# Performance work log

Hardware: AMD Instinct MI355X
Metric: run time of the kernel (lower is better)

## Reference

```python
import jax, jax.numpy as jnp
import numpy as np

N_U, N_I, E = 500000, 50000, 1000000
H, C = 4, 32  # heads, per-head channels


def _seg_softmax(e, dst, n_dst):
    # e: [E, H] edge scores, softmax over edges sharing the same destination
    m = jax.ops.segment_max(e, dst, num_segments=n_dst)
    ex = jnp.exp(e - m[dst])
    s = jax.ops.segment_sum(ex, dst, num_segments=n_dst)
    return ex / (s[dst] + 1e-16)


def _gatv2(xl, xr, src, dst, att, bias, n_dst, edge_feat=None):
    # GATv2 bipartite message passing (PyG semantics, no self-loops for bipartite).
    # xl: [N_src,H,C] transformed source, xr: [N_dst,H,C] transformed destination
    h = xl[src] + xr[dst]                      # [E,H,C] gather + add
    if edge_feat is not None:
        h = h + edge_feat                      # [E,H,C]
    e = jnp.sum(jax.nn.leaky_relu(h, 0.2) * att, axis=-1)   # [E,H]
    alpha = _seg_softmax(e, dst, n_dst)                      # [E,H]
    out = jax.ops.segment_sum(alpha[..., None] * xl[src], dst, num_segments=n_dst)
    return out.reshape(n_dst, H * C) + bias    # concat heads + bias


def setup_inputs() -> dict:
    key = jax.random.key(0)
    ks = iter(jax.random.split(key, 32))
    p = lambda *s: jax.random.normal(next(ks), s, dtype=jnp.float32) * 0.05
    inp = {
        "customer_x": jax.random.normal(next(ks), (N_U, 101), dtype=jnp.float32),
        "fund_x": jax.random.normal(next(ks), (N_I, 1), dtype=jnp.float32),
        "edge_attr": jax.random.uniform(next(ks), (E, 3), dtype=jnp.float32),
        "edge_src": jax.random.randint(next(ks), (E,), 0, N_U),
        "edge_dst": jax.random.randint(next(ks), (E,), 0, N_I),
        # input projections
        "user_W": p(101, 32), "user_b": jnp.zeros((32,), jnp.float32),
        "item_W": p(1, 32),   "item_b": jnp.zeros((32,), jnp.float32),
        # conv1: GATv2Conv((32,32), 32, heads=4, edge_dim=3)
        "c1_Wl": p(32, H * C), "c1_bl": jnp.zeros((H * C,), jnp.float32),
        "c1_Wr": p(32, H * C), "c1_br": jnp.zeros((H * C,), jnp.float32),
        "c1_We": p(3, H * C),
        "c1_att": p(H, C), "c1_bias": jnp.zeros((H * C,), jnp.float32),
        # conv2: GATv2Conv((128,32), 32, heads=4), called without edge_attr
        "c2_Wl": p(H * C, H * C), "c2_bl": jnp.zeros((H * C,), jnp.float32),
        "c2_Wr": p(32, H * C),    "c2_br": jnp.zeros((H * C,), jnp.float32),
        "c2_att": p(H, C), "c2_bias": jnp.zeros((H * C,), jnp.float32),
        # classifier MLP: 128 -> 64 -> 1
        "cls_W1": p(128, 64), "cls_b1": jnp.zeros((64,), jnp.float32),
        "cls_W2": p(64, 1),   "cls_b2": jnp.zeros((1,), jnp.float32),
    }
    return inp


def reference(customer_x, fund_x, edge_attr, edge_src, edge_dst,
              user_W, user_b, item_W, item_b,
              c1_Wl, c1_bl, c1_Wr, c1_br, c1_We, c1_att, c1_bias,
              c2_Wl, c2_bl, c2_Wr, c2_br, c2_att, c2_bias,
              cls_W1, cls_b1, cls_W2, cls_b2):
    user_x = customer_x @ user_W + user_b            # [N_U,32]
    item_x = fund_x @ item_W + item_b                # [N_I,32]
    # conv1: customer -> fund (dst = fund)
    xl1 = (user_x @ c1_Wl + c1_bl).reshape(N_U, H, C)
    xr1 = (item_x @ c1_Wr + c1_br).reshape(N_I, H, C)
    ef1 = (edge_attr @ c1_We).reshape(E, H, C)
    item_h = jax.nn.relu(_gatv2(xl1, xr1, edge_src, edge_dst, c1_att, c1_bias, N_I, ef1))
    # conv2: fund -> customer (edge_index flipped, no edge_attr)
    xl2 = (item_h @ c2_Wl + c2_bl).reshape(N_I, H, C)
    xr2 = (user_x @ c2_Wr + c2_br).reshape(N_U, H, C)
    user_h = _gatv2(xl2, xr2, edge_dst, edge_src, c2_att, c2_bias, N_U)  # [N_U,128]
    # anomaly classifier
    hid = jax.nn.relu(user_h @ cls_W1 + cls_b1)
    scores = jax.nn.sigmoid(hid @ cls_W2 + cls_b2)   # [N_U,1]
    return scores
```

## Files before the change

kernel.cpp:

```cpp
#include <hip/hip_runtime.h>
#include <cstdint>
#include <cstddef>

#define NU 500000
#define NI 50000
#define NE 1000000
#define HC 128
#define NH 4

typedef __attribute__((ext_vector_type(8))) short bf16x8;
typedef __attribute__((ext_vector_type(4))) float f32x4;

union frag_u { bf16x8 v; unsigned int u[4]; };

__device__ __forceinline__ unsigned int pack_bf2(float x, float y) {
    unsigned int r;
    asm("v_cvt_pk_bf16_f32 %0, %1, %2" : "=v"(r) : "v"(x), "v"(y));
    return r;
}
__device__ __forceinline__ float2 unpack_bf2(unsigned int v) {
    return make_float2(__uint_as_float(v << 16),
                       __uint_as_float(v & 0xffff0000u));
}
__device__ __forceinline__ unsigned short pack_bf1(float x) {
    unsigned int b = __float_as_uint(x);
    b += 0x7fffu + ((b >> 16) & 1u);
    return (unsigned short)(b >> 16);
}

__device__ __forceinline__ float head_reduce(float p) {
    p += __shfl_xor(p, 8, 16);
    p += __shfl_xor(p, 4, 16);
    p += __shfl_xor(p, 2, 16);
    p += __shfl_xor(p, 1, 16);
    return p;
}

__global__ void wprep(const float* __restrict__ user_W, const float* __restrict__ user_b,
                      const float* __restrict__ c1_Wl, const float* __restrict__ c1_bl,
                      const float* __restrict__ c2_Wr, const float* __restrict__ c2_br,
                      const float* __restrict__ c2_Wl, unsigned short* __restrict__ Bp)
{
    const int t = blockIdx.x * 256 + threadIdx.x;
    const int mat = t >> 14;
    const int k = (t >> 7) & 127;
    const int n = t & 127;
    float val = 0.f;
    if (mat == 2) {
        val = c2_Wl[k * 128 + n];
    } else {
        const float* W2 = mat ? c2_Wr : c1_Wl;
        if (k < 101) {
            for (int q = 0; q < 32; ++q) val = fmaf(user_W[k * 32 + q], W2[q * 128 + n], val);
        } else if (k == 101) {
            for (int q = 0; q < 32; ++q) val = fmaf(user_b[q], W2[q * 128 + n], val);
            val += (mat ? c2_br : c1_bl)[n];
        }
    }
    const int fi = (mat * 8 + (n >> 4)) * 4 + (k >> 5);
    const int lane_ = (n & 15) + ((k >> 3) & 3) * 16;
    Bp[(size_t)fi * 512 + lane_ * 8 + (k & 7)] = pack_bf1(val);
}

__global__ void w1prep(const float* __restrict__ W1, unsigned short* __restrict__ Bp1)
{
    const int t = blockIdx.x * 256 + threadIdx.x;
    const int k = t >> 6;
    const int n = t & 63;
    const float val = W1[k * 64 + n];
    const int fi = (n >> 4) * 4 + (k >> 5);
    const int lane_ = (n & 15) + ((k >> 3) & 3) * 16;
    Bp1[(size_t)fi * 512 + lane_ * 8 + (k & 7)] = pack_bf1(val);
}

__global__ void wvbb_prep(const float* __restrict__ item_W, const float* __restrict__ item_b,
                          const float* __restrict__ c1_Wr, const float* __restrict__ c1_br,
                          float* __restrict__ wvbb)
{
    const int j = threadIdx.x;
    if (j >= 128) return;
    float wv = 0.f, bb = 0.f;
    for (int q = 0; q < 32; ++q) {
        wv = fmaf(item_W[q], c1_Wr[q * 128 + j], wv);
        bb = fmaf(item_b[q], c1_Wr[q * 128 + j], bb);
    }
    wvbb[j] = wv;
    wvbb[128 + j] = bb + c1_br[j];
}

__global__ __launch_bounds__(256)
void mfma_user_scatter(const float* __restrict__ cx, const unsigned short* __restrict__ Bp,
                       unsigned short* __restrict__ outL, unsigned short* __restrict__ outR,
                       int M, int nub,
                       const int* __restrict__ src, const int* __restrict__ dst,
                       const float* __restrict__ eattr,
                       const int* __restrict__ offU, const int* __restrict__ offI,
                       const int* __restrict__ rankU, const int* __restrict__ rankI,
                       int* __restrict__ sFund, uint4* __restrict__ sE1, int E, int nscat)
{
    __shared__ float xs[64 * 108];

    if (blockIdx.x < nscat) {
        const int bid = blockIdx.x;
        for (int i = bid * 256 + threadIdx.x; i < E; i += nscat * 256) {
            const int s = src[i];
            const int d = dst[i];
            const float a0 = eattr[3 * (size_t)i];
            const float a1 = eattr[3 * (size_t)i + 1];
            const float a2 = eattr[3 * (size_t)i + 2];
            const int p1 = offI[d] + rankI[i];
            const int p2 = offU[s] + rankU[i];
            sE1[p1] = make_uint4((unsigned int)s, __float_as_uint(a0),
                                 __float_as_uint(a1), __float_as_uint(a2));
            sFund[p2] = d;
        }
        return;
    }

    const int tid = threadIdx.x;
    const int lane = tid & 63;
    const int wid = tid >> 6;
    const int rowblk = (blockIdx.x - nscat) * 64;
    const int rows = min(64, M - rowblk);

    const float* srcp = cx + (size_t)rowblk * 101;
    const int total = rows * 101;
    for (int i = tid; i < total; i += 256) {
        const int r = i / 101;
        const int c = i - r * 101;
        xs[r * 108 + c] = srcp[i];
    }
    __syncthreads();

    const int rowbase = wid * 16;
    if (rowbase >= rows) return;
    const int row = lane & 15;
    const int chunk = lane >> 4;
    const float* rowp = xs + (rowbase + row) * 108;

    frag_u a[4];
    #pragma unroll
    for (int ks = 0; ks < 3; ++ks) {
        const int kb = ks * 32 + chunk * 8;
        const float4 p = *(const float4*)(rowp + kb);
        const float4 q = *(const float4*)(rowp + kb + 4);
        a[ks].u[0] = pack_bf2(p.x, p.y);
        a[ks].u[1] = pack_bf2(p.z, p.w);
        a[ks].u[2] = pack_bf2(q.x, q.y);
        a[ks].u[3] = pack_bf2(q.z, q.w);
    }
    {
        float v0 = 0.f, v1 = 0.f, v2 = 0.f, v3 = 0.f, v4 = 0.f, v5 = 0.f;
        if (chunk == 0) {
            const float4 p = *(const float4*)(rowp + 96);
            v0 = p.x; v1 = p.y; v2 = p.z; v3 = p.w;
            v4 = rowp[100];
            v5 = 1.0f;
        }
        a[3].u[0] = pack_bf2(v0, v1);
        a[3].u[1] = pack_bf2(v2, v3);
        a[3].u[2] = pack_bf2(v4, v5);
        a[3].u[3] = 0u;
    }

    unsigned short* xpo = (unsigned short*)(xs + (size_t)wid * 16 * 108);

    const bf16x8* bfr = (const bf16x8*)Bp;
    #pragma unroll
    for (int mat = 0; mat < 2; ++mat) {
        unsigned short* outp = mat ? outR : outL;
        #pragma unroll
        for (int nf = 0; nf < 8; ++nf) {
            f32x4 acc = {0.f, 0.f, 0.f, 0.f};
            const int fi = (mat * 8 + nf) * 4;
            acc = __builtin_amdgcn_mfma_f32_16x16x32_bf16(a[0].v, bfr[(fi + 0) * 64 + lane], acc, 0, 0, 0);
            acc = __builtin_amdgcn_mfma_f32_16x16x32_bf16(a[1].v, bfr[(fi + 1) * 64 + lane], acc, 0, 0, 0);
            acc = __builtin_amdgcn_mfma_f32_16x16x32_bf16(a[2].v, bfr[(fi + 2) * 64 + lane], acc, 0, 0, 0);
            acc = __builtin_amdgcn_mfma_f32_16x16x32_bf16(a[3].v, bfr[(fi + 3) * 64 + lane], acc, 0, 0, 0);
            const int col = nf * 16 + row;
            #pragma unroll
            for (int j = 0; j < 4; ++j)
                xpo[(chunk * 4 + j) * 140 + col] = pack_bf1(acc[j]);
        }
        #pragma unroll
        for (int i = 0; i < 4; ++i) {
            const int r = i * 4 + chunk;
            const bf16x8 v = *(const bf16x8*)&xpo[r * 140 + row * 8];
            *(bf16x8*)(outp + (size_t)(rowblk + rowbase + r) * 128 + row * 8) = v;
        }
    }
}

__global__ __launch_bounds__(256)
void mfma_xl2(const float* __restrict__ X, const unsigned short* __restrict__ Bp,
              const float* __restrict__ bias, unsigned short* __restrict__ outp, int M)
{
    const int lane = threadIdx.x & 63;
    const int wt = (blockIdx.x * blockDim.x + threadIdx.x) >> 6;
    const int rowbase = wt * 16;
    if (rowbase >= M) return;
    const int chunk = lane >> 4;
    const float* rowp = X + (size_t)(rowbase + (lane & 15)) * 128;

    frag_u a[4];
    #pragma unroll
    for (int ks = 0; ks < 4; ++ks) {
        const int kb = ks * 32 + chunk * 8;
        const float4 p = *(const float4*)(rowp + kb);
        const float4 q = *(const float4*)(rowp + kb + 4);
        a[ks].u[0] = pack_bf2(p.x, p.y);
        a[ks].u[1] = pack_bf2(p.z, p.w);
        a[ks].u[2] = pack_bf2(q.x, q.y);
        a[ks].u[3] = pack_bf2(q.z, q.w);
    }

    const bf16x8* bfr = (const bf16x8*)Bp;
    #pragma unroll
    for (int nf = 0; nf < 8; ++nf) {
        f32x4 acc = {0.f, 0.f, 0.f, 0.f};
        const int fi = (16 + nf) * 4;
        acc = __builtin_amdgcn_mfma_f32_16x16x32_bf16(a[0].v, bfr[(fi + 0) * 64 + lane], acc, 0, 0, 0);
        acc = __builtin_amdgcn_mfma_f32_16x16x32_bf16(a[1].v, bfr[(fi + 1) * 64 + lane], acc, 0, 0, 0);
        acc = __builtin_amdgcn_mfma_f32_16x16x32_bf16(a[2].v, bfr[(fi + 2) * 64 + lane], acc, 0, 0, 0);
        acc = __builtin_amdgcn_mfma_f32_16x16x32_bf16(a[3].v, bfr[(fi + 3) * 64 + lane], acc, 0, 0, 0);
        const int col = nf * 16 + (lane & 15);
        const float bv = bias[col];
        #pragma unroll
        for (int j = 0; j < 4; ++j)
            outp[(size_t)(rowbase + chunk * 4 + j) * 128 + col] = pack_bf1(acc[j] + bv);
    }
}

__global__ void hist_rank(const int* __restrict__ src, const int* __restrict__ dst,
                          int* __restrict__ cntU, int* __restrict__ cntI,
                          int* __restrict__ rankU, int* __restrict__ rankI, int E)
{
    for (int i = blockIdx.x * blockDim.x + threadIdx.x; i < E;
         i += gridDim.x * blockDim.x) {
        rankU[i] = atomicAdd(&cntU[src[i]], 1);
        rankI[i] = atomicAdd(&cntI[dst[i]], 1);
    }
}

__global__ void scan_blocks(const int* __restrict__ in, int* __restrict__ out,
                            int* __restrict__ blockSums, int n)
{
    __shared__ int lds[256];
    const int tid = threadIdx.x;
    const int base = blockIdx.x * 1024 + tid * 4;
    int v[4];
    #pragma unroll
    for (int j = 0; j < 4; ++j) { int idx = base + j; v[j] = (idx < n) ? in[idx] : 0; }
    int t = v[0] + v[1] + v[2] + v[3];
    lds[tid] = t;
    __syncthreads();
    for (int off = 1; off < 256; off <<= 1) {
        int x = (tid >= off) ? lds[tid - off] : 0;
        __syncthreads();
        lds[tid] += x;
        __syncthreads();
    }
    int excl = lds[tid] - t;
    if (tid == 255 && blockSums) blockSums[blockIdx.x] = lds[255];
    int run = excl;
    #pragma unroll
    for (int j = 0; j < 4; ++j) {
        int idx = base + j;
        if (idx < n) out[idx] = run;
        run += v[j];
    }
}

__global__ void scan_add(int* __restrict__ out, const int* __restrict__ bss, int n)
{
    const int add = bss[blockIdx.x];
    const int base = blockIdx.x * 1024 + threadIdx.x * 4;
    #pragma unroll
    for (int j = 0; j < 4; ++j) { int idx = base + j; if (idx < n) out[idx] += add; }
}

__device__ __forceinline__ void conv1_edge(uint4 e, unsigned int vbits, float2 vr,
                                           float2 av, float2 w0, float2 w1, float2 w2,
                                           float& acc0, float& acc1, float& s)
{
    const float2 vl = unpack_bf2(vbits);
    const float e0 = __uint_as_float(e.y);
    const float e1 = __uint_as_float(e.z);
    const float e2 = __uint_as_float(e.w);
    float h0 = vl.x + vr.x + e0 * w0.x + e1 * w1.x + e2 * w2.x;
    float h1 = vl.y + vr.y + e0 * w0.y + e1 * w1.y + e2 * w2.y;
    h0 = h0 > 0.f ? h0 : 0.2f * h0;
    h1 = h1 > 0.f ? h1 : 0.2f * h1;
    const float p = head_reduce(h0 * av.x + h1 * av.y);
    const float ex = __expf(p);
    acc0 = fmaf(ex, vl.x, acc0);
    acc1 = fmaf(ex, vl.y, acc1);
    s += ex;
}

__global__ void conv1_fused(const unsigned int* __restrict__ xl,
                            const float* __restrict__ fund_x,
                            const float* __restrict__ wvbb,
                            const int* __restrict__ offI, const int* __restrict__ cnt,
                            const uint4* __restrict__ sE,
                            const float* __restrict__ We, const float* __restrict__ att,
                            const float* __restrict__ bias,
                            float* __restrict__ outF, int ndst)
{
    const int tid = threadIdx.x;
    const int lane = tid & 63;
    const int wid = tid >> 6;
    const int d = blockIdx.x * 4 + wid;
    if (d >= ndst) return;

    const int ch = lane * 2;
    const float2 av = *(const float2*)(att + ch);
    const float2 w0 = *(const float2*)(We + ch);
    const float2 w1 = *(const float2*)(We + HC + ch);
    const float2 w2 = *(const float2*)(We + 2 * HC + ch);
    const float2 bv = *(const float2*)(bias + ch);

    const float fx = fund_x[d];
    const float2 wv = *(const float2*)(wvbb + ch);
    const float2 bb = *(const float2*)(wvbb + 128 + ch);
    const float2 vr = make_float2(fmaf(fx, wv.x, bb.x), fmaf(fx, wv.y, bb.y));

    const int start = offI[d];
    const int end = start + cnt[d];

    float acc0 = 0.f, acc1 = 0.f, s = 0.f;
    int pos = start;
    for (; pos + 8 <= end; pos += 8) {
        uint4 e[8];
        unsigned int v[8];
        #pragma unroll
        for (int j = 0; j < 8; ++j) e[j] = sE[pos + j];
        #pragma unroll
        for (int j = 0; j < 8; ++j) v[j] = xl[(size_t)e[j].x * 64 + lane];
        #pragma unroll
        for (int j = 0; j < 8; ++j)
            conv1_edge(e[j], v[j], vr, av, w0, w1, w2, acc0, acc1, s);
    }
    for (; pos + 4 <= end; pos += 4) {
        uint4 e[4];
        unsigned int v[4];
        #pragma unroll
        for (int j = 0; j < 4; ++j) e[j] = sE[pos + j];
        #pragma unroll
        for (int j = 0; j < 4; ++j) v[j] = xl[(size_t)e[j].x * 64 + lane];
        #pragma unroll
        for (int j = 0; j < 4; ++j)
            conv1_edge(e[j], v[j], vr, av, w0, w1, w2, acc0, acc1, s);
    }
    for (; pos < end; ++pos) {
        const uint4 e = sE[pos];
        const unsigned int v = xl[(size_t)e.x * 64 + lane];
        conv1_edge(e, v, vr, av, w0, w1, w2, acc0, acc1, s);
    }
    const float inv = 1.f / (s + 1e-16f);
    const float o0 = fmaxf(acc0 * inv + bv.x, 0.f);
    const float o1 = fmaxf(acc1 * inv + bv.y, 0.f);
    *(float2*)(outF + (size_t)d * HC + ch) = make_float2(o0, o1);
}

__device__ __forceinline__ void conv2_edge(unsigned int vbits, float2 vr, float2 av,
                                           float& acc0, float& acc1, float& s)
{
    const float2 vl = unpack_bf2(vbits);
    float h0 = vl.x + vr.x;
    float h1 = vl.y + vr.y;
    h0 = h0 > 0.f ? h0 : 0.2f * h0;
    h1 = h1 > 0.f ? h1 : 0.2f * h1;
    const float p = head_reduce(h0 * av.x + h1 * av.y);
    const float ex = __expf(p);
    acc0 = fmaf(ex, vl.x, acc0);
    acc1 = fmaf(ex, vl.y, acc1);
    s += ex;
}

__global__ __launch_bounds__(256)
void conv2_cls(const unsigned int* __restrict__ xl2,
               const unsigned int* __restrict__ xr2,
               const int* __restrict__ offU, const int* __restrict__ cnt,
               const int* __restrict__ sFund,
               const float* __restrict__ att, const float* __restrict__ cbias,
               const unsigned short* __restrict__ Bp1,
               const float* __restrict__ b1, const float* __restrict__ W2,
               const float* __restrict__ b2,
               float* __restrict__ out, int nusr)
{
    __shared__ unsigned short xs[4][16][136];

    const int lane = threadIdx.x & 63;
    const int wid = threadIdx.x >> 6;
    const int wt = (blockIdx.x * blockDim.x + threadIdx.x) >> 6;
    const int u0 = wt * 16;
    if (u0 >= nusr) return;

    const int ch = lane * 2;
    const float2 av = *(const float2*)(att + ch);
    const float2 bv = *(const float2*)(cbias + ch);

    int so = 0, ctv = 0;
    if (lane < 16) {
        so = offU[u0 + lane];
        ctv = cnt[u0 + lane];
    }
    const int eo = so + ctv;
    const int S = __builtin_amdgcn_readlane(so, 0);
    const int E = __builtin_amdgcn_readlane(eo, 15);

    int u = 0;
    int end_u = __builtin_amdgcn_readlane(eo, 0);
    unsigned int vrb_next = xr2[(size_t)(u0 + 1) * 64 + lane];
    float2 vr = unpack_bf2(xr2[(size_t)u0 * 64 + lane]);
    float acc0 = 0.f, acc1 = 0.f, s = 0.f;

    #define FINALIZE() {                                                        \
        const float inv = 1.f / (s + 1e-16f);                                   \
        *(unsigned int*)&xs[wid][u][ch] = pack_bf2(acc0 * inv + bv.x,           \
                                                   acc1 * inv + bv.y);          \
        acc0 = acc1 = s = 0.f;                                                  \
        ++u;                                                                    \
        if (u < 16) {                                                           \
            end_u = __builtin_amdgcn_readlane(eo, u);                           \
            vr = unpack_bf2(vrb_next);                                          \
            if (u + 1 < 16) vrb_next = xr2[(size_t)(u0 + u + 1) * 64 + lane];   \
        }                                                                       \
    }

    int pos = S;
    while (pos < E) {
        const int f0 = sFund[pos];
        const int f1 = (pos + 1 < E) ? sFund[pos + 1] : f0;
        const int f2 = (pos + 2 < E) ? sFund[pos + 2] : f0;
        const int f3 = (pos + 3 < E) ? sFund[pos + 3] : f0;
        const unsigned int v0 = xl2[(size_t)f0 * 64 + lane];
        const unsigned int v1 = xl2[(size_t)f1 * 64 + lane];
        const unsigned int v2 = xl2[(size_t)f2 * 64 + lane];
        const unsigned int v3 = xl2[(size_t)f3 * 64 + lane];

        while (pos == end_u) FINALIZE();
        conv2_edge(v0, vr, av, acc0, acc1, s);
        if (pos + 1 < E) {
            while (pos + 1 == end_u) FINALIZE();
            conv2_edge(v1, vr, av, acc0, acc1, s);
        }
        if (pos + 2 < E) {
            while (pos + 2 == end_u) FINALIZE();
            conv2_edge(v2, vr, av, acc0, acc1, s);
        }
        if (pos + 3 < E) {
            while (pos + 3 == end_u) FINALIZE();
            conv2_edge(v3, vr, av, acc0, acc1, s);
        }
        pos += 4;
    }
    while (u < 16) FINALIZE();
    #undef FINALIZE

    const int row = lane & 15;
    const int chunk = lane >> 4;
    bf16x8 a[4];
    #pragma unroll
    for (int ks = 0; ks < 4; ++ks)
        a[ks] = *(const bf16x8*)&xs[wid][row][ks * 32 + chunk * 8];

    const bf16x8* bfr = (const bf16x8*)Bp1;
    float racc[4] = {0.f, 0.f, 0.f, 0.f};
    #pragma unroll
    for (int g = 0; g < 4; ++g) {
        f32x4 acc = {0.f, 0.f, 0.f, 0.f};
        const int fi = g * 4;
        acc = __builtin_amdgcn_mfma_f32_16x16x32_bf16(a[0], bfr[(fi + 0) * 64 + lane], acc, 0, 0, 0);
        acc = __builtin_amdgcn_mfma_f32_16x16x32_bf16(a[1], bfr[(fi + 1) * 64 + lane], acc, 0, 0, 0);
        acc = __builtin_amdgcn_mfma_f32_16x16x32_bf16(a[2], bfr[(fi + 2) * 64 + lane], acc, 0, 0, 0);
        acc = __builtin_amdgcn_mfma_f32_16x16x32_bf16(a[3], bfr[(fi + 3) * 64 + lane], acc, 0, 0, 0);
        const int col = g * 16 + row;
        const float b1v = b1[col];
        const float w2v = W2[col];
        #pragma unroll
        for (int j = 0; j < 4; ++j)
            racc[j] = fmaf(fmaxf(acc[j] + b1v, 0.f), w2v, racc[j]);
    }
    #pragma unroll
    for (int j = 0; j < 4; ++j) {
        racc[j] += __shfl_xor(racc[j], 1, 16);
        racc[j] += __shfl_xor(racc[j], 2, 16);
        racc[j] += __shfl_xor(racc[j], 4, 16);
        racc[j] += __shfl_xor(racc[j], 8, 16);
    }
    if (row == 0) {
        const float b2v = b2[0];
        #pragma unroll
        for (int j = 0; j < 4; ++j) {
            const int r = u0 + chunk * 4 + j;
            if (r < nusr) out[r] = 1.f / (1.f + expf(-(racc[j] + b2v)));
        }
    }
}

extern "C" void kernel_launch(void* const* d_in, const int* in_sizes, int n_in,
                              void* d_out, int out_size, void* d_ws, size_t ws_size,
                              hipStream_t stream)
{
    const float* customer_x = (const float*)d_in[0];
    const float* fund_x     = (const float*)d_in[1];
    const float* edge_attr  = (const float*)d_in[2];
    const int*   edge_src   = (const int*)d_in[3];
    const int*   edge_dst   = (const int*)d_in[4];
    const float* user_W = (const float*)d_in[5];
    const float* user_b = (const float*)d_in[6];
    const float* item_W = (const float*)d_in[7];
    const float* item_b = (const float*)d_in[8];
    const float* c1_Wl  = (const float*)d_in[9];
    const float* c1_bl  = (const float*)d_in[10];
    const float* c1_Wr  = (const float*)d_in[11];
    const float* c1_br  = (const float*)d_in[12];
    const float* c1_We  = (const float*)d_in[13];
    const float* c1_att = (const float*)d_in[14];
    const float* c1_bias= (const float*)d_in[15];
    const float* c2_Wl  = (const float*)d_in[16];
    const float* c2_bl  = (const float*)d_in[17];
    const float* c2_Wr  = (const float*)d_in[18];
    const float* c2_br  = (const float*)d_in[19];
    const float* c2_att = (const float*)d_in[20];
    const float* c2_bias= (const float*)d_in[21];
    const float* cls_W1 = (const float*)d_in[22];
    const float* cls_b1 = (const float*)d_in[23];
    const float* cls_W2 = (const float*)d_in[24];
    const float* cls_b2 = (const float*)d_in[25];
    float* out = (float*)d_out;

    float* ws = (float*)d_ws;
    size_t off = 0;
    unsigned short* B1 = (unsigned short*)(ws + off); off += (size_t)NU * 64;
    unsigned short* B2 = (unsigned short*)(ws + off); off += (size_t)NU * 64;
    float* F = ws + off; off += (size_t)NI * HC;
    unsigned short* G = (unsigned short*)(ws + off); off += (size_t)NI * 64;
    int* cnt1  = (int*)(ws + off); off += NI;
    int* off1  = (int*)(ws + off); off += NI;
    int* cnt2  = (int*)(ws + off); off += NU;
    int* off2  = (int*)(ws + off); off += NU;
    int* bs    = (int*)(ws + off); off += 1024;
    int* bss   = (int*)(ws + off); off += 1024;
    uint4* sE1 = (uint4*)(ws + off); off += (size_t)NE * 4;
    int* sFund = (int*)(ws + off); off += NE;
    int* rankU = (int*)(ws + off); off += NE;
    int* rankI = (int*)(ws + off); off += NE;
    unsigned short* Bp = (unsigned short*)(ws + off); off += 12288 + 256;
    unsigned short* Bp1 = (unsigned short*)(ws + off); off += 4096 + 256;
    float* wvbb = ws + off; off += 256;

    hipMemsetAsync(cnt1, 0, NI * sizeof(int), stream);
    hipMemsetAsync(cnt2, 0, NU * sizeof(int), stream);

    hist_rank<<<1024, 256, 0, stream>>>(edge_src, edge_dst, cnt2, cnt1,
                                        rankU, rankI, NE);
    const int nb1 = (NI + 1023) / 1024;
    const int nb2 = (NU + 1023) / 1024;
    scan_blocks<<<nb1, 256, 0, stream>>>(cnt1, off1, bs, NI);
    scan_blocks<<<1,   256, 0, stream>>>(bs, bss, nullptr, nb1);
    scan_add<<<nb1, 256, 0, stream>>>(off1, bss, NI);
    scan_blocks<<<nb2, 256, 0, stream>>>(cnt2, off2, bs, NU);
    scan_blocks<<<1,   256, 0, stream>>>(bs, bss, nullptr, nb2);
    scan_add<<<nb2, 256, 0, stream>>>(off2, bss, NU);

    wprep<<<192, 256, 0, stream>>>(user_W, user_b, c1_Wl, c1_bl,
                                   c2_Wr, c2_br, c2_Wl, Bp);
    w1prep<<<32, 256, 0, stream>>>(cls_W1, Bp1);
    wvbb_prep<<<1, 128, 0, stream>>>(item_W, item_b, c1_Wr, c1_br, wvbb);

    const int nub = (NU + 63) / 64;
    const int nscat = 2048;
    mfma_user_scatter<<<nscat + nub, 256, 0, stream>>>(
        customer_x, Bp, B1, B2, NU, nub,
        edge_src, edge_dst, edge_attr, off2, off1, rankU, rankI,
        sFund, sE1, NE, nscat);

    conv1_fused<<<NI / 4, 256, 0, stream>>>((const unsigned int*)B1, fund_x, wvbb,
                                            off1, cnt1, sE1,
                                            c1_We, c1_att, c1_bias, F, NI);

    mfma_xl2<<<(NI / 16 + 3) / 4, 256, 0, stream>>>(F, Bp, c2_bl, G, NI);

    const int waves2 = (NU + 15) / 16;
    conv2_cls<<<(waves2 + 3) / 4, 256, 0, stream>>>(
        (const unsigned int*)G, (const unsigned int*)B2, off2, cnt2, sFund,
        c2_att, c2_bias, Bp1, cls_b1, cls_W2, cls_b2, out, NU);
}
```

Before: 531.1 us.

## Split user projection GEMM across histogram and scatter kernels to overlap work

The user-feature MFMA projection is split into two halves. The first half runs as extra blocks inside the histogram/rank kernel, and the remaining rows run alongside the edge scatter kernel. Weight prep is moved ahead of the histogram so the packed weights are ready. The aim is to fill the GPU while the atomic-bound histogram and scatter phases run, at the cost of more LDS-heavy blocks competing with the atomics.

```diff
diff --git a/kernel.cpp b/kernel.cpp
--- a/kernel.cpp
+++ b/kernel.cpp
@@ -88,39 +88,14 @@
     wvbb[128 + j] = bb + c1_br[j];
 }
 
-__global__ __launch_bounds__(256)
-void mfma_user_scatter(const float* __restrict__ cx, const unsigned short* __restrict__ Bp,
-                       unsigned short* __restrict__ outL, unsigned short* __restrict__ outR,
-                       int M, int nub,
-                       const int* __restrict__ src, const int* __restrict__ dst,
-                       const float* __restrict__ eattr,
-                       const int* __restrict__ offU, const int* __restrict__ offI,
-                       const int* __restrict__ rankU, const int* __restrict__ rankI,
-                       int* __restrict__ sFund, uint4* __restrict__ sE1, int E, int nscat)
-{
-    __shared__ float xs[64 * 108];
-
-    if (blockIdx.x < nscat) {
-        const int bid = blockIdx.x;
-        for (int i = bid * 256 + threadIdx.x; i < E; i += nscat * 256) {
-            const int s = src[i];
-            const int d = dst[i];
-            const float a0 = eattr[3 * (size_t)i];
-            const float a1 = eattr[3 * (size_t)i + 1];
-            const float a2 = eattr[3 * (size_t)i + 2];
-            const int p1 = offI[d] + rankI[i];
-            const int p2 = offU[s] + rankU[i];
-            sE1[p1] = make_uint4((unsigned int)s, __float_as_uint(a0),
-                                 __float_as_uint(a1), __float_as_uint(a2));
-            sFund[p2] = d;
-        }
-        return;
-    }
-
-    const int tid = threadIdx.x;
+__device__ __forceinline__
+void mfma_role(float* xs, const float* __restrict__ cx,
+               const unsigned short* __restrict__ Bp,
+               unsigned short* __restrict__ outL, unsigned short* __restrict__ outR,
+               int M, int rowblk, int tid)
+{
     const int lane = tid & 63;
     const int wid = tid >> 6;
-    const int rowblk = (blockIdx.x - nscat) * 64;
     const int rows = min(64, M - rowblk);
 
     const float* srcp = cx + (size_t)rowblk * 101;
@@ -192,6 +167,56 @@
 }
 
 __global__ __launch_bounds__(256)
+void hist_mfma(const int* __restrict__ src, const int* __restrict__ dst,
+               int* __restrict__ cntU, int* __restrict__ cntI,
+               int* __restrict__ rankU, int* __restrict__ rankI, int E, int nhist,
+               const float* __restrict__ cx, const unsigned short* __restrict__ Bp,
+               unsigned short* __restrict__ outL, unsigned short* __restrict__ outR, int M)
+{
+    __shared__ float xs[64 * 108];
+
+    if (blockIdx.x < nhist) {
+        for (int i = blockIdx.x * 256 + threadIdx.x; i < E; i += nhist * 256) {
+            rankU[i] = atomicAdd(&cntU[src[i]], 1);
+            rankI[i] = atomicAdd(&cntI[dst[i]], 1);
+        }
+        return;
+    }
+    mfma_role(xs, cx, Bp, outL, outR, M, (blockIdx.x - nhist) * 64, threadIdx.x);
+}
+
+__global__ __launch_bounds__(256)
+void scat_mfma(const int* __restrict__ src, const int* __restrict__ dst,
+               const float* __restrict__ eattr,
+               const int* __restrict__ offU, const int* __restrict__ offI,
+               const int* __restrict__ rankU, const int* __restrict__ rankI,
+               int* __restrict__ sFund, uint4* __restrict__ sE1, int E, int nscat,
+               const float* __restrict__ cx, const unsigned short* __restrict__ Bp,
+               unsigned short* __restrict__ outL, unsigned short* __restrict__ outR,
+               int M, int rowoff)
+{
+    __shared__ float xs[64 * 108];
+
+    if (blockIdx.x < nscat) {
+        for (int i = blockIdx.x * 256 + threadIdx.x; i < E; i += nscat * 256) {
+            const int s = src[i];
+            const int d = dst[i];
+            const float a0 = eattr[3 * (size_t)i];
+            const float a1 = eattr[3 * (size_t)i + 1];
+            const float a2 = eattr[3 * (size_t)i + 2];
+            const int p1 = offI[d] + rankI[i];
+            const int p2 = offU[s] + rankU[i];
+            sE1[p1] = make_uint4((unsigned int)s, __float_as_uint(a0),
+                                 __float_as_uint(a1), __float_as_uint(a2));
+            sFund[p2] = d;
+        }
+        return;
+    }
+    mfma_role(xs, cx, Bp, outL, outR, M,
+              rowoff + (blockIdx.x - nscat) * 64, threadIdx.x);
+}
+
+__global__ __launch_bounds__(256)
 void mfma_xl2(const float* __restrict__ X, const unsigned short* __restrict__ Bp,
               const float* __restrict__ bias, unsigned short* __restrict__ outp, int M)
 {
@@ -228,17 +253,6 @@
         #pragma unroll
         for (int j = 0; j < 4; ++j)
             outp[(size_t)(rowbase + chunk * 4 + j) * 128 + col] = pack_bf1(acc[j] + bv);
-    }
-}
-
-__global__ void hist_rank(const int* __restrict__ src, const int* __restrict__ dst,
-                          int* __restrict__ cntU, int* __restrict__ cntI,
-                          int* __restrict__ rankU, int* __restrict__ rankI, int E)
-{
-    for (int i = blockIdx.x * blockDim.x + threadIdx.x; i < E;
-         i += gridDim.x * blockDim.x) {
-        rankU[i] = atomicAdd(&cntU[src[i]], 1);
-        rankI[i] = atomicAdd(&cntI[dst[i]], 1);
     }
 }
 
@@ -555,8 +569,16 @@
     hipMemsetAsync(cnt1, 0, NI * sizeof(int), stream);
     hipMemsetAsync(cnt2, 0, NU * sizeof(int), stream);
 
-    hist_rank<<<1024, 256, 0, stream>>>(edge_src, edge_dst, cnt2, cnt1,
-                                        rankU, rankI, NE);
+    wprep<<<192, 256, 0, stream>>>(user_W, user_b, c1_Wl, c1_bl,
+                                   c2_Wr, c2_br, c2_Wl, Bp);
+    w1prep<<<32, 256, 0, stream>>>(cls_W1, Bp1);
+    wvbb_prep<<<1, 128, 0, stream>>>(item_W, item_b, c1_Wr, c1_br, wvbb);
+
+    const int nubA = 3906;
+    hist_mfma<<<1024 + nubA, 256, 0, stream>>>(
+        edge_src, edge_dst, cnt2, cnt1, rankU, rankI, NE, 1024,
+        customer_x, Bp, B1, B2, nubA * 64);
+
     const int nb1 = (NI + 1023) / 1024;
     const int nb2 = (NU + 1023) / 1024;
     scan_blocks<<<nb1, 256, 0, stream>>>(cnt1, off1, bs, NI);
@@ -566,17 +588,12 @@
     scan_blocks<<<1,   256, 0, stream>>>(bs, bss, nullptr, nb2);
     scan_add<<<nb2, 256, 0, stream>>>(off2, bss, NU);
 
-    wprep<<<192, 256, 0, stream>>>(user_W, user_b, c1_Wl, c1_bl,
-                                   c2_Wr, c2_br, c2_Wl, Bp);
-    w1prep<<<32, 256, 0, stream>>>(cls_W1, Bp1);
-    wvbb_prep<<<1, 128, 0, stream>>>(item_W, item_b, c1_Wr, c1_br, wvbb);
-
-    const int nub = (NU + 63) / 64;
-    const int nscat = 2048;
-    mfma_user_scatter<<<nscat + nub, 256, 0, stream>>>(
-        customer_x, Bp, B1, B2, NU, nub,
+    const int rowoff = nubA * 64;
+    const int nubB = (NU - rowoff + 63) / 64;
+    scat_mfma<<<2048 + nubB, 256, 0, stream>>>(
         edge_src, edge_dst, edge_attr, off2, off1, rankU, rankI,
-        sFund, sE1, NE, nscat);
+        sFund, sE1, NE, 2048,
+        customer_x, Bp, B1, B2, NU, rowoff);
 
     conv1_fused<<<NI / 4, 256, 0, stream>>>((const unsigned int*)B1, fund_x, wvbb,
                                             off1, cnt1, sE1,
```

Result: no change. 528.8 us (-0.4%).
